# Kernel tuning notes

Measured on AMD Instinct MI355X. Metric: run time of the kernel, lower is better.

Reference implementation:

```python
import jax, jax.numpy as jnp
import numpy as np

CH, HEADS, DH, NMEM, GROUPS, EPS = 128, 4, 32, 4, 32, 1e-5
HID = HEADS * DH

def group_norm(x, w, b):
    # x: [B,C,D,H,W], normalize per group of channels over (C//G, D, H, W)
    B, C = x.shape[0], x.shape[1]
    xg = x.reshape(B, GROUPS, -1)
    mu = xg.mean(axis=-1, keepdims=True)
    var = xg.var(axis=-1, keepdims=True)
    xg = (xg - mu) * jax.lax.rsqrt(var + EPS)
    x = xg.reshape(x.shape)
    return x * w[None, :, None, None, None] + b[None, :, None, None, None]

def setup_inputs() -> dict:
    key = jax.random.key(0)
    ks = jax.random.split(key, 8)
    B, D, H, W = 2, 16, 64, 64
    x = jax.random.normal(ks[0], (B, CH, D, H, W), dtype=jnp.float32)
    norm1_w = jnp.ones((CH,), jnp.float32)
    norm1_b = jnp.zeros((CH,), jnp.float32)
    w_qkv = jax.random.normal(ks[1], (3 * HID, CH), dtype=jnp.float32) * (CH ** -0.5)
    mem_kv = jax.random.normal(ks[2], (2, HEADS, DH, NMEM), dtype=jnp.float32)
    w_out = jax.random.normal(ks[3], (CH, HID), dtype=jnp.float32) * (HID ** -0.5)
    b_out = jnp.zeros((CH,), jnp.float32)
    norm2_w = jnp.ones((CH,), jnp.float32)
    norm2_b = jnp.zeros((CH,), jnp.float32)
    return {"x": x, "norm1_w": norm1_w, "norm1_b": norm1_b, "w_qkv": w_qkv,
            "mem_kv": mem_kv, "w_out": w_out, "b_out": b_out,
            "norm2_w": norm2_w, "norm2_b": norm2_b}

def reference(x, norm1_w, norm1_b, w_qkv, mem_kv, w_out, b_out, norm2_w, norm2_b):
    B, C, D, H, W = x.shape
    n = D * H * W
    scale = DH ** -0.5
    xn = group_norm(x, norm1_w, norm1_b)
    # 1x1x1 conv == channel matmul: [B,3*HID,n]
    qkv = jnp.einsum('oc,bcn->bon', w_qkv, xn.reshape(B, C, n))
    qkv = qkv.reshape(B, 3, HEADS, DH, n)
    q, k, v = qkv[:, 0], qkv[:, 1], qkv[:, 2]  # [B,HEADS,DH,n]
    mk = jnp.broadcast_to(mem_kv[0][None], (B, HEADS, DH, NMEM))
    mv = jnp.broadcast_to(mem_kv[1][None], (B, HEADS, DH, NMEM))
    k = jnp.concatenate([mk, k], axis=-1)
    v = jnp.concatenate([mv, v], axis=-1)
    q = jax.nn.softmax(q, axis=-2) * scale   # over dim_head
    k = jax.nn.softmax(k, axis=-1)           # over sequence
    context = jnp.einsum('bhdn,bhen->bhde', k, v)  # [B,HEADS,DH,DH]
    out = jnp.einsum('bhde,bhdn->bhen', context, q)  # [B,HEADS,DH,n]
    out = out.reshape(B, HID, D, H, W)
    out = jnp.einsum('oc,bcdhw->bodhw', w_out, out) + b_out[None, :, None, None, None]
    return group_norm(out, norm2_w, norm2_b)
```

## Files before the change

kernel.cpp:

```cpp
#include <hip/hip_runtime.h>
#include <math.h>

#define CH     128
#define EPSV   1e-5f
#define SCALE  0.17677669529663687f
#define GSIZE  262144.0f

typedef short bf16x8 __attribute__((ext_vector_type(8)));
typedef short bf16x4 __attribute__((ext_vector_type(4)));
typedef float f32x4  __attribute__((ext_vector_type(4)));

__device__ __forceinline__ unsigned cvtpk(float lo, float hi) {
    unsigned r;
    asm("v_cvt_pk_bf16_f32 %0, %1, %2" : "=v"(r) : "v"(lo), "v"(hi));
    return r;
}
__device__ __forceinline__ bf16x4 pk4(unsigned p01, unsigned p23) {
    union { unsigned u[2]; bf16x4 v; } t;
    t.u[0] = p01; t.u[1] = p23;
    return t.v;
}
__device__ __forceinline__ bf16x8 pk8(unsigned a, unsigned b, unsigned c, unsigned d) {
    union { unsigned u[4]; bf16x8 v; } t;
    t.u[0] = a; t.u[1] = b; t.u[2] = c; t.u[3] = d;
    return t.v;
}
__device__ __forceinline__ unsigned short f2bf(float f) {
    unsigned u = __float_as_uint(f);
    u += 0x7FFF + ((u >> 16) & 1);
    return (unsigned short)(u >> 16);
}
__device__ __forceinline__ float bf2f(unsigned short s) {
    return __uint_as_float(((unsigned)s) << 16);
}

__global__ __launch_bounds__(256) void gn_partial(const float* __restrict__ x,
                                                  float* __restrict__ part) {
    __shared__ float s1[256], s2[256];
    int t = threadIdx.x;
    const float4* xp = (const float4*)(x + (size_t)blockIdx.x * 8192);
    float s = 0.f, q = 0.f;
#pragma unroll
    for (int i = 0; i < 8; ++i) {
        float4 v = xp[t + 256 * i];
        s += v.x + v.y + v.z + v.w;
        q += v.x * v.x + v.y * v.y + v.z * v.z + v.w * v.w;
    }
    s1[t] = s; s2[t] = q;
    __syncthreads();
    for (int st = 128; st > 0; st >>= 1) {
        if (t < st) { s1[t] += s1[t + st]; s2[t] += s2[t + st]; }
        __syncthreads();
    }
    if (t == 0) { part[2 * blockIdx.x] = s1[0]; part[2 * blockIdx.x + 1] = s2[0]; }
}

__global__ void prep1(const float* __restrict__ part, float* __restrict__ mu, float* __restrict__ rs) {
    int t = threadIdx.x;
    float s = 0.f, q = 0.f;
    for (int i = 0; i < 32; ++i) { s += part[2*(t*32+i)]; q += part[2*(t*32+i)+1]; }
    float m = s * (1.f / GSIZE);
    float v = q * (1.f / GSIZE) - m * m;
    mu[t] = m; rs[t] = rsqrtf(v + EPSV);
}

__global__ __launch_bounds__(256) void kv_pass(const float* __restrict__ x,
        const float* __restrict__ w_qkv,
        const float* __restrict__ n1w, const float* __restrict__ n1b,
        const float* __restrict__ mu, const float* __restrict__ rs,
        float* __restrict__ part_kv) {
    __shared__ short xk[16*64*8];
    __shared__ short kvstage[8*256*8];
    __shared__ float betas[256];
    int tid = threadIdx.x;
    int l = tid & 63, w = tid >> 6;
    int ncol = l & 15, kg = l >> 4;
    int b = blockIdx.x >> 8;
    int h = w;

    bf16x8 afrag[4][4];
    float bsum[4] = {0.f, 0.f, 0.f, 0.f};
#pragma unroll
    for (int ks = 0; ks < 4; ++ks) {
        float a0[8], b0[8];
#pragma unroll
        for (int j = 0; j < 8; ++j) {
            int c = 8*kg + 32*ks + j;
            int fg = b*32 + (c >> 2);
            float av = rs[fg] * n1w[c];
            a0[j] = av;
            b0[j] = n1b[c] - mu[fg] * av;
        }
#pragma unroll
        for (int rt = 0; rt < 4; ++rt) {
            const float* p = w_qkv + (size_t)(128 + w*64 + 16*rt + ncol)*CH + 8*kg + 32*ks;
            float4 u0 = *(const float4*)p, u1 = *(const float4*)(p + 4);
            float wv[8] = {u0.x,u0.y,u0.z,u0.w,u1.x,u1.y,u1.z,u1.w};
            afrag[rt][ks] = pk8(cvtpk(wv[0]*a0[0], wv[1]*a0[1]), cvtpk(wv[2]*a0[2], wv[3]*a0[3]),
                                cvtpk(wv[4]*a0[4], wv[5]*a0[5]), cvtpk(wv[6]*a0[6], wv[7]*a0[7]));
#pragma unroll
            for (int j = 0; j < 8; ++j) bsum[rt] += wv[j] * b0[j];
        }
    }
#pragma unroll
    for (int rt = 0; rt < 4; ++rt) {
        bsum[rt] += __shfl_xor(bsum[rt], 16);
        bsum[rt] += __shfl_xor(bsum[rt], 32);
    }
    if (kg == 0) {
#pragma unroll
        for (int rt = 0; rt < 4; ++rt) betas[w*64 + 16*rt + ncol] = bsum[rt];
    }

    int nst = (tid & 15) * 4;
    int cst = (tid >> 4) * 8;

    f32x4 cc[2][2];
#pragma unroll
    for (int i = 0; i < 2; ++i)
#pragma unroll
    for (int j = 0; j < 2; ++j)
#pragma unroll
    for (int q = 0; q < 4; ++q) cc[i][j][q] = 0.f;
    float zacc[2] = {0.f, 0.f};

    float4 xv[8];
    {
        int n0 = ((blockIdx.x * 4) << 6) & 65535;
#pragma unroll
        for (int i = 0; i < 8; ++i)
            xv[i] = *(const float4*)(x + ((size_t)(b*CH + cst + i) << 16) + n0 + nst);
        const float* xf = (const float*)xv;
#pragma unroll
        for (int j = 0; j < 4; ++j)
            *(bf16x8*)&xk[((cst >> 3)*64 + nst + j) * 8] =
                pk8(cvtpk(xf[0*4+j], xf[1*4+j]), cvtpk(xf[2*4+j], xf[3*4+j]),
                    cvtpk(xf[4*4+j], xf[5*4+j]), cvtpk(xf[6*4+j], xf[7*4+j]));
    }

    for (int t4 = 0; t4 < 4; ++t4) {
        __syncthreads();

        f32x4 acc[4][4];
#pragma unroll
        for (int i = 0; i < 4; ++i)
#pragma unroll
        for (int j = 0; j < 4; ++j)
#pragma unroll
        for (int q = 0; q < 4; ++q) acc[i][j][q] = 0.f;

#pragma unroll
        for (int ks = 0; ks < 4; ++ks) {
            bf16x8 bfr[4];
#pragma unroll
            for (int ct = 0; ct < 4; ++ct)
                bfr[ct] = *(bf16x8*)&xk[((4*ks + kg)*64 + 16*ct + ncol) * 8];
#pragma unroll
            for (int rt = 0; rt < 4; ++rt)
#pragma unroll
            for (int ct = 0; ct < 4; ++ct)
                acc[rt][ct] = __builtin_amdgcn_mfma_f32_16x16x32_bf16(
                    afrag[rt][ks], bfr[ct], acc[rt][ct], 0, 0, 0);
        }

#pragma unroll
        for (int rt = 0; rt < 4; ++rt) {
            int lrow0 = w*64 + 16*rt + 4*kg;
            float be0 = betas[lrow0+0], be1 = betas[lrow0+1];
            float be2 = betas[lrow0+2], be3 = betas[lrow0+3];
#pragma unroll
            for (int ct = 0; ct < 4; ++ct) {
                float v0 = acc[rt][ct][0] + be0, v1 = acc[rt][ct][1] + be1;
                float v2 = acc[rt][ct][2] + be2, v3 = acc[rt][ct][3] + be3;
                if (w < 2) { v0 = __expf(v0); v1 = __expf(v1); v2 = __expf(v2); v3 = __expf(v3); }
                unsigned p01 = cvtpk(v0, v1), p23 = cvtpk(v2, v3);
                unsigned short sv[4] = {(unsigned short)p01, (unsigned short)(p01 >> 16),
                                        (unsigned short)p23, (unsigned short)(p23 >> 16)};
                int n = 16*ct + ncol;
#pragma unroll
                for (int q = 0; q < 4; ++q) {
                    int row = lrow0 + q;
                    int byteoff = ((n >> 3)*4096 + row*16 + (n & 7)*2) ^ (((row >> 2) & 3) << 4);
                    *(unsigned short*)((char*)kvstage + byteoff) = sv[q];
                }
            }
        }
        __syncthreads();

        if (t4 < 3) {
            int n0 = ((blockIdx.x * 4 + t4 + 1) << 6) & 65535;
#pragma unroll
            for (int i = 0; i < 8; ++i)
                xv[i] = *(const float4*)(x + ((size_t)(b*CH + cst + i) << 16) + n0 + nst);
        }

#pragma unroll
        for (int ks = 0; ks < 2; ++ks) {
            bf16x8 ak[2], bv[2];
#pragma unroll
            for (int rt = 0; rt < 2; ++rt) {
                int row = h*32 + 16*rt + ncol;
                int byteoff = ((4*ks + kg)*4096 + row*16) ^ (((row >> 2) & 3) << 4);
                ak[rt] = *(bf16x8*)((char*)kvstage + byteoff);
            }
#pragma unroll
            for (int ct = 0; ct < 2; ++ct) {
                int row = 128 + h*32 + 16*ct + ncol;
                int byteoff = ((4*ks + kg)*4096 + row*16) ^ (((row >> 2) & 3) << 4);
                bv[ct] = *(bf16x8*)((char*)kvstage + byteoff);
            }
#pragma unroll
            for (int rt = 0; rt < 2; ++rt)
#pragma unroll
            for (int j = 0; j < 8; ++j) zacc[rt] += bf2f((unsigned short)ak[rt][j]);
#pragma unroll
            for (int rt = 0; rt < 2; ++rt)
#pragma unroll
            for (int ct = 0; ct < 2; ++ct)
                cc[rt][ct] = __builtin_amdgcn_mfma_f32_16x16x32_bf16(
                    ak[rt], bv[ct], cc[rt][ct], 0, 0, 0);
        }

        if (t4 < 3) {
            const float* xf = (const float*)xv;
#pragma unroll
            for (int j = 0; j < 4; ++j)
                *(bf16x8*)&xk[((cst >> 3)*64 + nst + j) * 8] =
                    pk8(cvtpk(xf[0*4+j], xf[1*4+j]), cvtpk(xf[2*4+j], xf[3*4+j]),
                        cvtpk(xf[4*4+j], xf[5*4+j]), cvtpk(xf[6*4+j], xf[7*4+j]));
        }
    }

    float* dst = part_kv + (size_t)blockIdx.x * 4224;
#pragma unroll
    for (int rt = 0; rt < 2; ++rt)
#pragma unroll
    for (int ct = 0; ct < 2; ++ct)
#pragma unroll
    for (int q = 0; q < 4; ++q) {
        int d = 16*rt + 4*kg + q;
        int e = 16*ct + ncol;
        dst[h*1024 + d*32 + e] = cc[rt][ct][q];
    }
#pragma unroll
    for (int rt = 0; rt < 2; ++rt) {
        zacc[rt] += __shfl_xor(zacc[rt], 16);
        zacc[rt] += __shfl_xor(zacc[rt], 32);
    }
    if (kg == 0) {
        dst[4096 + h*32 + ncol]      = zacc[0];
        dst[4096 + h*32 + 16 + ncol] = zacc[1];
    }
}

__global__ __launch_bounds__(256) void reduce_ctx(const float* __restrict__ part_kv,
                                                  const float* __restrict__ mem_kv,
                                                  float* __restrict__ ctx, float* __restrict__ Z) {
    int gid = blockIdx.x * 256 + threadIdx.x;
    int oi = gid >> 2, sub = gid & 3;
    int b = oi / 4224;
    int e = oi - b * 4224;
    const float* p = part_kv + (size_t)b * 256 * 4224 + e;
    float s = 0.f;
    for (int i = sub; i < 256; i += 4) s += p[(size_t)i * 4224];
    s += __shfl_xor(s, 1);
    s += __shfl_xor(s, 2);
    if (sub == 0) {
        if (e < 4096) {
            int hh = e >> 10, d = (e >> 5) & 31, ee = e & 31;
            float init = 0.f;
            for (int m = 0; m < 4; ++m)
                init += expf(mem_kv[hh*128 + d*4 + m]) * mem_kv[512 + hh*128 + ee*4 + m];
            ctx[b*4096 + e] = init + s;
        } else {
            int d2 = e - 4096;
            float init = 0.f;
            for (int m = 0; m < 4; ++m) init += expf(mem_kv[d2*4 + m]);
            Z[b*128 + d2] = init + s;
        }
    }
}

template<bool BF16OUT>
__global__ __launch_bounds__(256) void out_pass(const float* __restrict__ x,
        const float* __restrict__ w_qkv,
        const float* __restrict__ n1w, const float* __restrict__ n1b,
        const float* __restrict__ mu, const float* __restrict__ rs,
        const float* __restrict__ ctx, const float* __restrict__ Z,
        const float* __restrict__ w_out, const float* __restrict__ b_out,
        float* __restrict__ out, unsigned short* __restrict__ outb,
        float* __restrict__ part2) {
    __shared__ short xk[16*64*8];
    __shared__ short pb[16*64*8];
    __shared__ float betasq[128];
    int tid = threadIdx.x;
    int l = tid & 63, w = tid >> 6;
    int ncol = l & 15, kg = l >> 4;
    int b = blockIdx.x >> 8;

    bf16x8 aq[2][4], aw[2][4];
    float bsq[2] = {0.f, 0.f};
#pragma unroll
    for (int ks = 0; ks < 4; ++ks) {
        float a0[8], b0[8];
#pragma unroll
        for (int j = 0; j < 8; ++j) {
            int c = 8*kg + 32*ks + j;
            int fg = b*32 + (c >> 2);
            float av = rs[fg] * n1w[c];
            a0[j] = av;
            b0[j] = n1b[c] - mu[fg] * av;
        }
#pragma unroll
        for (int rt = 0; rt < 2; ++rt) {
            const float* pq = w_qkv + (size_t)(32*w + 16*rt + ncol)*CH + 8*kg + 32*ks;
            const float* pw = w_out + (size_t)(32*w + 16*rt + ncol)*CH + 8*kg + 32*ks;
            float4 u0 = *(const float4*)pq, u1 = *(const float4*)(pq + 4);
            float4 v0 = *(const float4*)pw, v1 = *(const float4*)(pw + 4);
            float wq[8] = {u0.x,u0.y,u0.z,u0.w,u1.x,u1.y,u1.z,u1.w};
            float wo[8] = {v0.x,v0.y,v0.z,v0.w,v1.x,v1.y,v1.z,v1.w};
            aq[rt][ks] = pk8(cvtpk(wq[0]*a0[0], wq[1]*a0[1]), cvtpk(wq[2]*a0[2], wq[3]*a0[3]),
                             cvtpk(wq[4]*a0[4], wq[5]*a0[5]), cvtpk(wq[6]*a0[6], wq[7]*a0[7]));
            aw[rt][ks] = pk8(cvtpk(wo[0], wo[1]), cvtpk(wo[2], wo[3]),
                             cvtpk(wo[4], wo[5]), cvtpk(wo[6], wo[7]));
#pragma unroll
            for (int j = 0; j < 8; ++j) bsq[rt] += wq[j] * b0[j];
        }
    }
#pragma unroll
    for (int rt = 0; rt < 2; ++rt) {
        bsq[rt] += __shfl_xor(bsq[rt], 16);
        bsq[rt] += __shfl_xor(bsq[rt], 32);
    }
    if (kg == 0) {
#pragma unroll
        for (int rt = 0; rt < 2; ++rt) betasq[32*w + 16*rt + ncol] = bsq[rt];
    }

    bf16x8 actx[2];
#pragma unroll
    for (int rt = 0; rt < 2; ++rt) {
        bf16x8 f;
#pragma unroll
        for (int j = 0; j < 8; ++j) {
            int d = 8*kg + j;
            float cv = ctx[b*4096 + w*1024 + d*32 + 16*rt + ncol] / Z[b*128 + w*32 + d];
            f[j] = (short)f2bf(cv);
        }
        actx[rt] = f;
    }

    float bo[2][4];
#pragma unroll
    for (int rt = 0; rt < 2; ++rt)
#pragma unroll
    for (int q = 0; q < 4; ++q)
        bo[rt][q] = b_out[32*w + 16*rt + 4*kg + q];

    int nst = (tid & 15) * 4;
    int cst = (tid >> 4) * 8;
    float pgs[2] = {0.f, 0.f}, pgq[2] = {0.f, 0.f};
    float4 xv[8];

    {
        int n0 = (blockIdx.x << 8) & 65535;
#pragma unroll
        for (int i = 0; i < 8; ++i)
            xv[i] = *(const float4*)(x + ((size_t)(b*CH + cst + i) << 16) + n0 + nst);
        const float* xf = (const float*)xv;
#pragma unroll
        for (int j = 0; j < 4; ++j)
            *(bf16x8*)&xk[((cst >> 3)*64 + nst + j) * 8] =
                pk8(cvtpk(xf[0*4+j], xf[1*4+j]), cvtpk(xf[2*4+j], xf[3*4+j]),
                    cvtpk(xf[4*4+j], xf[5*4+j]), cvtpk(xf[6*4+j], xf[7*4+j]));
    }

    for (int t4 = 0; t4 < 4; ++t4) {
        int n0 = ((blockIdx.x*4 + t4) << 6) & 65535;
        __syncthreads();

        f32x4 acc[2][4];
#pragma unroll
        for (int i = 0; i < 2; ++i)
#pragma unroll
        for (int j = 0; j < 4; ++j)
#pragma unroll
        for (int q = 0; q < 4; ++q) acc[i][j][q] = 0.f;
#pragma unroll
        for (int ks = 0; ks < 4; ++ks) {
            bf16x8 bfr[4];
#pragma unroll
            for (int ct = 0; ct < 4; ++ct)
                bfr[ct] = *(bf16x8*)&xk[((4*ks + kg)*64 + 16*ct + ncol) * 8];
#pragma unroll
            for (int rt = 0; rt < 2; ++rt)
#pragma unroll
            for (int ct = 0; ct < 4; ++ct)
                acc[rt][ct] = __builtin_amdgcn_mfma_f32_16x16x32_bf16(
                    aq[rt][ks], bfr[ct], acc[rt][ct], 0, 0, 0);
        }

        {
            float be[2][4];
#pragma unroll
            for (int rt = 0; rt < 2; ++rt)
#pragma unroll
            for (int q = 0; q < 4; ++q) be[rt][q] = betasq[32*w + 16*rt + 4*kg + q];
            float sum[4];
#pragma unroll
            for (int ct = 0; ct < 4; ++ct) {
                float s = 0.f;
#pragma unroll
                for (int rt = 0; rt < 2; ++rt)
#pragma unroll
                for (int q = 0; q < 4; ++q) {
                    float e = __expf(acc[rt][ct][q] + be[rt][q]);
                    acc[rt][ct][q] = e;
                    s += e;
                }
                s += __shfl_xor(s, 16);
                s += __shfl_xor(s, 32);
                sum[ct] = SCALE / s;
            }
#pragma unroll
            for (int ct = 0; ct < 4; ++ct)
#pragma unroll
            for (int rt = 0; rt < 2; ++rt) {
                unsigned p01 = cvtpk(acc[rt][ct][0]*sum[ct], acc[rt][ct][1]*sum[ct]);
                unsigned p23 = cvtpk(acc[rt][ct][2]*sum[ct], acc[rt][ct][3]*sum[ct]);
                int row0 = w*32 + 16*rt + 4*kg;
                *(bf16x4*)&pb[((row0 >> 3)*64 + 16*ct + ncol)*8 + (row0 & 7)] = pk4(p01, p23);
            }
        }

        f32x4 hacc[2][4];
#pragma unroll
        for (int i = 0; i < 2; ++i)
#pragma unroll
        for (int j = 0; j < 4; ++j)
#pragma unroll
        for (int q = 0; q < 4; ++q) hacc[i][j][q] = 0.f;
        {
            bf16x8 bq[4];
#pragma unroll
            for (int ct = 0; ct < 4; ++ct)
                bq[ct] = *(bf16x8*)&pb[((w*4 + kg)*64 + 16*ct + ncol) * 8];
#pragma unroll
            for (int rt = 0; rt < 2; ++rt)
#pragma unroll
            for (int ct = 0; ct < 4; ++ct)
                hacc[rt][ct] = __builtin_amdgcn_mfma_f32_16x16x32_bf16(
                    actx[rt], bq[ct], hacc[rt][ct], 0, 0, 0);
        }

#pragma unroll
        for (int ct = 0; ct < 4; ++ct)
#pragma unroll
        for (int rt = 0; rt < 2; ++rt) {
            unsigned p01 = cvtpk(hacc[rt][ct][0], hacc[rt][ct][1]);
            unsigned p23 = cvtpk(hacc[rt][ct][2], hacc[rt][ct][3]);
            int row0 = w*32 + 16*rt + 4*kg;
            *(bf16x4*)&pb[((row0 >> 3)*64 + 16*ct + ncol)*8 + (row0 & 7)] = pk4(p01, p23);
        }
        __syncthreads();

        if (t4 < 3) {
            int n1 = ((blockIdx.x*4 + t4 + 1) << 6) & 65535;
#pragma unroll
            for (int i = 0; i < 8; ++i)
                xv[i] = *(const float4*)(x + ((size_t)(b*CH + cst + i) << 16) + n1 + nst);
        }

        f32x4 oacc[2][4];
#pragma unroll
        for (int i = 0; i < 2; ++i)
#pragma unroll
        for (int j = 0; j < 4; ++j)
#pragma unroll
        for (int q = 0; q < 4; ++q) oacc[i][j][q] = 0.f;
#pragma unroll
        for (int ks = 0; ks < 4; ++ks) {
            bf16x8 bfr[4];
#pragma unroll
            for (int ct = 0; ct < 4; ++ct)
                bfr[ct] = *(bf16x8*)&pb[((4*ks + kg)*64 + 16*ct + ncol) * 8];
#pragma unroll
            for (int rt = 0; rt < 2; ++rt)
#pragma unroll
            for (int ct = 0; ct < 4; ++ct)
                oacc[rt][ct] = __builtin_amdgcn_mfma_f32_16x16x32_bf16(
                    aw[rt][ks], bfr[ct], oacc[rt][ct], 0, 0, 0);
        }

#pragma unroll
        for (int rt = 0; rt < 2; ++rt)
#pragma unroll
        for (int ct = 0; ct < 4; ++ct)
#pragma unroll
        for (int q = 0; q < 4; ++q) {
            int c = 32*w + 16*rt + 4*kg + q;
            float o = oacc[rt][ct][q] + bo[rt][q];
            size_t idx = ((size_t)(b*CH + c) << 16) + n0 + 16*ct + ncol;
            if (BF16OUT) outb[idx] = f2bf(o);
            else         out[idx] = o;
            pgs[rt] += o;
            pgq[rt] += o*o;
        }

        if (t4 < 3) {
            const float* xf = (const float*)xv;
#pragma unroll
            for (int j = 0; j < 4; ++j)
                *(bf16x8*)&xk[((cst >> 3)*64 + nst + j) * 8] =
                    pk8(cvtpk(xf[0*4+j], xf[1*4+j]), cvtpk(xf[2*4+j], xf[3*4+j]),
                        cvtpk(xf[4*4+j], xf[5*4+j]), cvtpk(xf[6*4+j], xf[7*4+j]));
        }
    }

#pragma unroll
    for (int rt = 0; rt < 2; ++rt) {
        float gs = pgs[rt], gq = pgq[rt];
#pragma unroll
        for (int m = 1; m < 16; m <<= 1) {
            gs += __shfl_xor(gs, m);
            gq += __shfl_xor(gq, m);
        }
        if (ncol == 0) {
            int g = 8*w + 4*rt + kg;
            part2[blockIdx.x*64 + g*2 + 0] = gs;
            part2[blockIdx.x*64 + g*2 + 1] = gq;
        }
    }
}

__global__ __launch_bounds__(256) void reduce2(const float* __restrict__ part2,
                                               float* __restrict__ mu, float* __restrict__ rs) {
    __shared__ float s1[256], s2[256];
    int fg = blockIdx.x;
    int b = fg >> 5, g = fg & 31;
    int t = threadIdx.x;
    const float* p = part2 + ((size_t)(b*256 + t))*64 + g*2;
    s1[t] = p[0]; s2[t] = p[1];
    __syncthreads();
    for (int st = 128; st > 0; st >>= 1) {
        if (t < st) { s1[t] += s1[t + st]; s2[t] += s2[t + st]; }
        __syncthreads();
    }
    if (t == 0) {
        float m = s1[0] * (1.f / GSIZE);
        float v = s2[0] * (1.f / GSIZE) - m*m;
        mu[fg] = m; rs[fg] = rsqrtf(v + EPSV);
    }
}

__global__ __launch_bounds__(256) void gn_apply(float* __restrict__ y,
        const float* __restrict__ mu, const float* __restrict__ rs,
        const float* __restrict__ w2, const float* __restrict__ b2) {
    int bi = blockIdx.x, t = threadIdx.x;
    int c = (bi >> 3) & 127;
    int b = bi >> 10;
    int fg = b*32 + (c >> 2);
    float aa = rs[fg] * w2[c];
    float bb = b2[c] - mu[fg] * aa;
    float4* yp = (float4*)(y + (size_t)bi * 8192);
#pragma unroll
    for (int i = 0; i < 8; ++i) {
        float4 v = yp[t + 256*i];
        v.x = v.x*aa+bb; v.y = v.y*aa+bb; v.z = v.z*aa+bb; v.w = v.w*aa+bb;
        yp[t + 256*i] = v;
    }
}

__global__ __launch_bounds__(256) void gn_apply_bf16(const unsigned short* __restrict__ src,
        float* __restrict__ y,
        const float* __restrict__ mu, const float* __restrict__ rs,
        const float* __restrict__ w2, const float* __restrict__ b2) {
    int bi = blockIdx.x, t = threadIdx.x;
    int c = (bi >> 3) & 127;
    int b = bi >> 10;
    int fg = b*32 + (c >> 2);
    float aa = rs[fg] * w2[c];
    float bb = b2[c] - mu[fg] * aa;
    const ushort4* sp = (const ushort4*)(src + (size_t)bi * 8192);
    float4* yp = (float4*)(y + (size_t)bi * 8192);
#pragma unroll
    for (int i = 0; i < 8; ++i) {
        ushort4 u = sp[t + 256*i];
        float4 v;
        v.x = bf2f(u.x)*aa+bb; v.y = bf2f(u.y)*aa+bb;
        v.z = bf2f(u.z)*aa+bb; v.w = bf2f(u.w)*aa+bb;
        yp[t + 256*i] = v;
    }
}

extern "C" void kernel_launch(void* const* d_in, const int* in_sizes, int n_in,
                              void* d_out, int out_size, void* d_ws, size_t ws_size,
                              hipStream_t stream) {
    (void)in_sizes; (void)n_in; (void)out_size;
    const float* x      = (const float*)d_in[0];
    const float* n1w    = (const float*)d_in[1];
    const float* n1b    = (const float*)d_in[2];
    const float* w_qkv  = (const float*)d_in[3];
    const float* mem_kv = (const float*)d_in[4];
    const float* w_out  = (const float*)d_in[5];
    const float* b_out  = (const float*)d_in[6];
    const float* n2w    = (const float*)d_in[7];
    const float* n2b    = (const float*)d_in[8];
    float* out = (float*)d_out;
    float* ws  = (float*)d_ws;

    float* part1   = ws;
    float* mu1     = ws + 4096;
    float* rs1     = ws + 4160;
    float* ctx     = ws + 4224;
    float* Z       = ws + 12416;
    float* part2   = ws + 12672;
    float* mu2     = ws + 143744;
    float* rs2     = ws + 143808;
    float* part_kv = ws + 143872;
    const size_t base_floats = 143872 + (size_t)512*4224;
    unsigned short* outb = (unsigned short*)(ws + base_floats);
    const size_t need = base_floats*4 + (size_t)2*CH*65536*2;
    bool bf16path = ws_size >= need;

    gn_partial<<<2048, 256, 0, stream>>>(x, part1);
    prep1<<<1, 64, 0, stream>>>(part1, mu1, rs1);
    kv_pass<<<512, 256, 0, stream>>>(x, w_qkv, n1w, n1b, mu1, rs1, part_kv);
    reduce_ctx<<<132, 256, 0, stream>>>(part_kv, mem_kv, ctx, Z);
    if (bf16path) {
        out_pass<true><<<512, 256, 0, stream>>>(x, w_qkv, n1w, n1b, mu1, rs1, ctx, Z,
                                                w_out, b_out, out, outb, part2);
        reduce2<<<64, 256, 0, stream>>>(part2, mu2, rs2);
        gn_apply_bf16<<<2048, 256, 0, stream>>>(outb, out, mu2, rs2, n2w, n2b);
    } else {
        out_pass<false><<<512, 256, 0, stream>>>(x, w_qkv, n1w, n1b, mu1, rs1, ctx, Z,
                                                 w_out, b_out, out, outb, part2);
        reduce2<<<64, 256, 0, stream>>>(part2, mu2, rs2);
        gn_apply<<<2048, 256, 0, stream>>>(out, mu2, rs2, n2w, n2b);
    }
}
```

Measured before the change: 131.5 us.

## Double out_pass grid to 1024 blocks with two tiles each, drop x prefetch

The out_pass kernel now launches 1024 blocks, each processing two 64-column tiles instead of four, so more blocks are spread across the CUs. The register-held prefetch of the next x tile is removed and replaced by a synchronous load at the start of each tile, which frees registers. The output bias moves from registers to shared memory. reduce2 is updated to sum 512 partials per batch. The change trades load/compute overlap and more per-block setup (weight conversion, ctx loads) for higher occupancy and parallelism.

New measurement: 132.0 us. No clear change (+0.4%).

```diff
diff --git a/kernel.cpp b/kernel.cpp
--- a/kernel.cpp
+++ b/kernel.cpp
@@ -293,10 +293,11 @@
     __shared__ short xk[16*64*8];
     __shared__ short pb[16*64*8];
     __shared__ float betasq[128];
+    __shared__ float bos[128];
     int tid = threadIdx.x;
     int l = tid & 63, w = tid >> 6;
     int ncol = l & 15, kg = l >> 4;
-    int b = blockIdx.x >> 8;
+    int b = blockIdx.x >> 9;
 
     bf16x8 aq[2][4], aw[2][4];
     float bsq[2] = {0.f, 0.f};
@@ -336,6 +337,7 @@
 #pragma unroll
         for (int rt = 0; rt < 2; ++rt) betasq[32*w + 16*rt + ncol] = bsq[rt];
     }
+    if (l < 32) bos[w*32 + l] = b_out[w*32 + l];
 
     bf16x8 actx[2];
 #pragma unroll
@@ -350,33 +352,25 @@
         actx[rt] = f;
     }
 
-    float bo[2][4];
-#pragma unroll
-    for (int rt = 0; rt < 2; ++rt)
-#pragma unroll
-    for (int q = 0; q < 4; ++q)
-        bo[rt][q] = b_out[32*w + 16*rt + 4*kg + q];
-
     int nst = (tid & 15) * 4;
     int cst = (tid >> 4) * 8;
     float pgs[2] = {0.f, 0.f}, pgq[2] = {0.f, 0.f};
-    float4 xv[8];
-
-    {
-        int n0 = (blockIdx.x << 8) & 65535;
-#pragma unroll
-        for (int i = 0; i < 8; ++i)
-            xv[i] = *(const float4*)(x + ((size_t)(b*CH + cst + i) << 16) + n0 + nst);
-        const float* xf = (const float*)xv;
-#pragma unroll
-        for (int j = 0; j < 4; ++j)
-            *(bf16x8*)&xk[((cst >> 3)*64 + nst + j) * 8] =
-                pk8(cvtpk(xf[0*4+j], xf[1*4+j]), cvtpk(xf[2*4+j], xf[3*4+j]),
-                    cvtpk(xf[4*4+j], xf[5*4+j]), cvtpk(xf[6*4+j], xf[7*4+j]));
-    }
-
-    for (int t4 = 0; t4 < 4; ++t4) {
-        int n0 = ((blockIdx.x*4 + t4) << 6) & 65535;
+
+    for (int t2 = 0; t2 < 2; ++t2) {
+        int n0 = ((blockIdx.x*2 + t2) << 6) & 65535;
+
+        {
+            float4 xv[8];
+#pragma unroll
+            for (int i = 0; i < 8; ++i)
+                xv[i] = *(const float4*)(x + ((size_t)(b*CH + cst + i) << 16) + n0 + nst);
+            const float* xf = (const float*)xv;
+#pragma unroll
+            for (int j = 0; j < 4; ++j)
+                *(bf16x8*)&xk[((cst >> 3)*64 + nst + j) * 8] =
+                    pk8(cvtpk(xf[0*4+j], xf[1*4+j]), cvtpk(xf[2*4+j], xf[3*4+j]),
+                        cvtpk(xf[4*4+j], xf[5*4+j]), cvtpk(xf[6*4+j], xf[7*4+j]));
+        }
         __syncthreads();
 
         f32x4 acc[2][4];
@@ -464,13 +458,6 @@
         }
         __syncthreads();
 
-        if (t4 < 3) {
-            int n1 = ((blockIdx.x*4 + t4 + 1) << 6) & 65535;
-#pragma unroll
-            for (int i = 0; i < 8; ++i)
-                xv[i] = *(const float4*)(x + ((size_t)(b*CH + cst + i) << 16) + n1 + nst);
-        }
-
         f32x4 oacc[2][4];
 #pragma unroll
         for (int i = 0; i < 2; ++i)
@@ -499,21 +486,12 @@
 #pragma unroll
         for (int q = 0; q < 4; ++q) {
             int c = 32*w + 16*rt + 4*kg + q;
-            float o = oacc[rt][ct][q] + bo[rt][q];
+            float o = oacc[rt][ct][q] + bos[c];
             size_t idx = ((size_t)(b*CH + c) << 16) + n0 + 16*ct + ncol;
             if (BF16OUT) outb[idx] = f2bf(o);
             else         out[idx] = o;
             pgs[rt] += o;
             pgq[rt] += o*o;
-        }
-
-        if (t4 < 3) {
-            const float* xf = (const float*)xv;
-#pragma unroll
-            for (int j = 0; j < 4; ++j)
-                *(bf16x8*)&xk[((cst >> 3)*64 + nst + j) * 8] =
-                    pk8(cvtpk(xf[0*4+j], xf[1*4+j]), cvtpk(xf[2*4+j], xf[3*4+j]),
-                        cvtpk(xf[4*4+j], xf[5*4+j]), cvtpk(xf[6*4+j], xf[7*4+j]));
         }
     }
 
@@ -539,8 +517,12 @@
     int fg = blockIdx.x;
     int b = fg >> 5, g = fg & 31;
     int t = threadIdx.x;
-    const float* p = part2 + ((size_t)(b*256 + t))*64 + g*2;
-    s1[t] = p[0]; s2[t] = p[1];
+    float s = 0.f, q = 0.f;
+    for (int i = t; i < 512; i += 256) {
+        const float* p = part2 + ((size_t)(b*512 + i))*64 + g*2;
+        s += p[0]; q += p[1];
+    }
+    s1[t] = s; s2[t] = q;
     __syncthreads();
     for (int st = 128; st > 0; st >>= 1) {
         if (t < st) { s1[t] += s1[t + st]; s2[t] += s2[t + st]; }
@@ -628,13 +610,13 @@
     kv_pass<<<512, 256, 0, stream>>>(x, w_qkv, n1w, n1b, mu1, rs1, part_kv);
     reduce_ctx<<<132, 256, 0, stream>>>(part_kv, mem_kv, ctx, Z);
     if (bf16path) {
-        out_pass<true><<<512, 256, 0, stream>>>(x, w_qkv, n1w, n1b, mu1, rs1, ctx, Z,
-                                                w_out, b_out, out, outb, part2);
+        out_pass<true><<<1024, 256, 0, stream>>>(x, w_qkv, n1w, n1b, mu1, rs1, ctx, Z,
+                                                 w_out, b_out, out, outb, part2);
         reduce2<<<64, 256, 0, stream>>>(part2, mu2, rs2);
         gn_apply_bf16<<<2048, 256, 0, stream>>>(outb, out, mu2, rs2, n2w, n2b);
     } else {
-        out_pass<false><<<512, 256, 0, stream>>>(x, w_qkv, n1w, n1b, mu1, rs1, ctx, Z,
-                                                 w_out, b_out, out, outb, part2);
+        out_pass<false><<<1024, 256, 0, stream>>>(x, w_qkv, n1w, n1b, mu1, rs1, ctx, Z,
+                                                  w_out, b_out, out, outb, part2);
         reduce2<<<64, 256, 0, stream>>>(part2, mu2, rs2);
         gn_apply<<<2048, 256, 0, stream>>>(out, mu2, rs2, n2w, n2b);
     }
```
